# Kernel tuning notes

Hardware: AMD Instinct MI355X
Metric: run time of the kernel (lower is better)

## Reference

```python
import jax, jax.numpy as jnp
import numpy as np

H, W, C, R, N = 200, 200, 256, 1024, 300


def _mlp(f, W1, b1, W2, b2):
    # Linear -> ReLU -> Linear, applied per pixel
    return jax.nn.relu(f @ W1 + b1) @ W2 + b2


def setup_inputs() -> dict:
    key = jax.random.key(0)
    ks = jax.random.split(key, 16)
    s = 0.02
    inp = {
        'x': jax.random.normal(ks[0], (C, H, W), jnp.float32),
        'masks': jax.random.uniform(ks[1], (H, W, N)) < 0.5,
        'labels': jax.random.randint(ks[2], (N,), 0, 3),  # 0=point,1=line,2=circle
    }
    i = 3
    for p in ('p', 'l', 'c'):
        inp[f'W{p}1'] = s * jax.random.normal(ks[i], (C, R), jnp.float32); i += 1
        inp[f'b{p}1'] = jnp.zeros((R,), jnp.float32)
        inp[f'W{p}2'] = s * jax.random.normal(ks[i], (R, R), jnp.float32); i += 1
        inp[f'b{p}2'] = jnp.zeros((R,), jnp.float32)
    return inp


def reference(x, masks, labels, Wp1, bp1, Wp2, bp2, Wl1, bl1, Wl2, bl2, Wc1, bc1, Wc2, bc2):
    feat = jnp.transpose(x, (1, 2, 0))  # [H, W, C]
    # Apply each label-specific MLP densely over the feature map: [3, H, W, R]
    ys = jnp.stack([
        _mlp(feat, Wp1, bp1, Wp2, bp2),
        _mlp(feat, Wl1, bl1, Wl2, bl2),
        _mlp(feat, Wc1, bc1, Wc2, bc2),
    ], axis=0)
    mf = masks.astype(feat.dtype)                       # [H, W, N]
    sums = jnp.einsum('hwn,khwr->nkr', mf, ys)          # masked sums per node per MLP
    counts = jnp.sum(mf, axis=(0, 1))                   # [N] pixels per mask
    means = sums / counts[:, None, None]                # [N, 3, R]
    # pick the MLP branch matching each node's label -> [N, R]
    return means[jnp.arange(means.shape[0]), labels]
```

## Files before the change

### kernel.cpp

```cpp
#include <hip/hip_runtime.h>

typedef unsigned short u16;
typedef unsigned int   u32;

using bf16x8 = __attribute__((ext_vector_type(8))) __bf16;
using f32x4  = __attribute__((ext_vector_type(4))) float;

__device__ __forceinline__ float bf2f(u16 h){ return __uint_as_float(((u32)h) << 16); }
__device__ __forceinline__ u16 f2bf(float f){
    u32 u = __float_as_uint(f);
    u32 r = u + 0x7FFFu + ((u >> 16) & 1u);
    return (u16)(r >> 16);
}

__device__ __forceinline__ void async16(const void* g, void* l){
    __builtin_amdgcn_global_load_lds(
        (const __attribute__((address_space(1))) unsigned int*)g,
        (__attribute__((address_space(3))) unsigned int*)l, 16, 0, 0);
}
__device__ __forceinline__ bf16x8 cvt8(uint4 v){
    union { uint4 u; bf16x8 b; } c; c.u = v; return c.b;
}

__global__ void probe_and_perm(const void* x, const void* masks, int* flags,
                               const int* labels, int* slot_of_node,
                               int* node_of_slot, int* ovf_flag)
{
    if (blockIdx.x == 0){
        int l = threadIdx.x;
        if (l < 64){
            const u16* hx = (const u16*)x;
            int e0 = (hx[l] >> 7) & 0xFF;
            int e1 = (hx[l + 64] >> 7) & 0xFF;
            unsigned long long b0 = __ballot(e0 >= 100 && e0 <= 140);
            unsigned long long b1 = __ballot(e1 >= 100 && e1 <= 140);
            int cnt = __popcll(b0) + __popcll(b1);
            const u32* w  = (const u32*)masks;
            const u16* hm = (const u16*)masks;
            u32 v = w[l];
            unsigned long long i32bad = __ballot(v > 1u);
            unsigned long long f32bad = __ballot(v != 0u && v != 0x3F800000u);
            u16 h0 = hm[l], h1 = hm[l + 64];
            unsigned long long bfbad =
                __ballot((h0 != 0 && h0 != 0x3F80) || (h1 != 0 && h1 != 0x3F80));
            if (l == 0){
                flags[0] = (cnt >= 100) ? 1 : 0;
                int md = 0;
                if (!i32bad) md = 1; else if (!f32bad) md = 3; else if (!bfbad) md = 2;
                flags[1] = md;
            }
        }
        return;
    }
    __shared__ int lab[300];
    __shared__ unsigned char sp[300];
    int t = threadIdx.x;
    for (int idx = t; idx < 512; idx += 320) node_of_slot[idx] = -1;
    if (t < 300) lab[t] = labels[t];
    __syncthreads();
    int r = 0;
    if (t < 300){
        int k = lab[t];
        for (int j = 0; j < t; j++) r += (lab[j] == k);
        sp[t] = (r >= 128) ? 1 : 0;
    }
    __syncthreads();
    if (t < 300){
        int slot;
        if (!sp[t]) slot = lab[t] * 128 + r;
        else {
            int so = 0;
            for (int j = 0; j < t; j++) so += sp[j];
            slot = 384 + so;
        }
        slot_of_node[t] = slot;
        node_of_slot[slot] = t;
    }
    if (t == 0){
        int tot = 0;
        for (int j = 0; j < 300; j++) tot += sp[j];
        *ovf_flag = tot;
    }
}

__global__ void prep_combo(const void* x,
    const void* w10, const void* w11, const void* w12,
    const void* w20, const void* w21, const void* w22,
    const void* bb10, const void* bb11, const void* bb12,
    const void* bb20, const void* bb21, const void* bb22,
    u16* feat, u16* B1T, u16* W2T, float* b1f, float* b2f, const int* flags)
{
    __shared__ float tile[32][33];
    const int id = blockIdx.x;
    const bool isbf = (flags[0] != 0);
    const int tid = threadIdx.x;
    const int tx = tid & 31, ty = tid >> 5;

    const void* src; u16* d; int I, J, ldd, i0, j0;
    if (id < 10016){
        int fx = id % 1252, fy = id / 1252;
        src = x; d = feat; I = 256; J = 40000; ldd = 256;
        j0 = fx * 32; i0 = fy * 32;
    } else if (id < 10016 + 768){
        int idx = id - 10016;
        int z = idx / 256, r2 = idx % 256;
        src = (z == 0) ? w10 : (z == 1) ? w11 : w12;
        d = B1T + (size_t)z * 1024 * 256;
        I = 256; J = 1024; ldd = 256;
        j0 = (r2 % 32) * 32; i0 = (r2 / 32) * 32;
    } else if (id < 10016 + 768 + 3072){
        int idx = id - 10016 - 768;
        int z = idx / 1024, r2 = idx % 1024;
        src = (z == 0) ? w20 : (z == 1) ? w21 : w22;
        d = W2T + (size_t)z * 1024 * 1024;
        I = 1024; J = 1024; ldd = 1024;
        j0 = (r2 % 32) * 32; i0 = (r2 / 32) * 32;
    } else {
        int idx = (id - 10016 - 768 - 3072) * 256 + tid;
        if (idx < 3072){
            int k = idx >> 10, r2 = idx & 1023;
            const void* p1 = (k == 0) ? bb10 : (k == 1) ? bb11 : bb12;
            const void* p2 = (k == 0) ? bb20 : (k == 1) ? bb21 : bb22;
            b1f[idx] = isbf ? bf2f(((const u16*)p1)[r2]) : ((const float*)p1)[r2];
            b2f[idx] = isbf ? bf2f(((const u16*)p2)[r2]) : ((const float*)p2)[r2];
        }
        return;
    }
    #pragma unroll
    for (int s = 0; s < 32; s += 8){
        int i = i0 + ty + s, j = j0 + tx;
        float v = 0.f;
        if (j < J){
            size_t ix = (size_t)i * J + j;
            v = isbf ? bf2f(((const u16*)src)[ix]) : ((const float*)src)[ix];
        }
        tile[ty + s][tx] = v;
    }
    __syncthreads();
    #pragma unroll
    for (int s = 0; s < 32; s += 8){
        int j = j0 + ty + s, i = i0 + tx;
        d[(size_t)j * ldd + i] = f2bf(tile[tx][ty + s]);
    }
}

__global__ void trans_mask_count(const void* src, u16* dst,
                                 const int* slot_of_node, float* counts,
                                 const int* flags)
{
    constexpr int NN_ = 300, P_ = 40000, LDP = 40064;
    __shared__ u16 tile[128][33];
    __shared__ int slt[32];
    const int p0 = blockIdx.x * 128, n0 = blockIdx.y * 32;
    const int tid = threadIdx.x;
    const int md = flags[1];
    if (tid < 32) slt[tid] = (n0 + tid < NN_) ? slot_of_node[n0 + tid] : -1;

    if (md == 0){
        const unsigned char* s8 = (const unsigned char*)src;
        const int tx = tid & 7, ty = tid >> 3;
        #pragma unroll
        for (int rep = 0; rep < 4; rep++){
            const int p = p0 + rep * 32 + ty;
            const int nb = n0 + tx * 4;
            u32 w = 0;
            if (p < P_){
                if (nb + 3 < NN_)
                    w = *(const u32*)(s8 + (size_t)p * NN_ + nb);
                else {
                    for (int b = 0; b < 4; b++)
                        if (nb + b < NN_)
                            w |= (u32)s8[(size_t)p * NN_ + nb + b] << (8 * b);
                }
            }
            #pragma unroll
            for (int b = 0; b < 4; b++)
                tile[rep * 32 + ty][tx * 4 + b] =
                    ((w >> (8 * b)) & 0xFFu) ? (u16)0x3F80 : (u16)0;
        }
    } else {
        #pragma unroll
        for (int it = 0; it < 16; it++){
            const int e = tid + it * 256;
            const int n_in = e & 31, p_in = e >> 5;
            const int p = p0 + p_in, n = n0 + n_in;
            u16 v = 0;
            if (p < P_ && n < NN_){
                size_t idx = (size_t)p * NN_ + n;
                bool on;
                if (md == 1)      on = ((const int*)src)[idx] != 0;
                else if (md == 2) on = ((const u16*)src)[idx] != 0;
                else              on = ((const float*)src)[idx] != 0.f;
                v = on ? (u16)0x3F80 : (u16)0;
            }
            tile[p_in][n_in] = v;
        }
    }
    __syncthreads();

    #pragma unroll
    for (int half = 0; half < 2; half++){
        const int row = tid >> 3;
        const int pos = (tid & 7) + half * 8;
        const int slot = slt[row];
        if (slot >= 0){
            union { u16 h[8]; uint4 v; } tmp;
            #pragma unroll
            for (int j = 0; j < 8; j++) tmp.h[j] = tile[pos * 8 + j][row];
            *reinterpret_cast<uint4*>(&dst[(size_t)slot * LDP + p0 + pos * 8]) = tmp.v;
        }
    }
    if (tid < 32){
        const int slot = slt[tid];
        if (slot >= 0){
            int c = 0;
            for (int p = 0; p < 128; p++) c += (tile[p][tid] != 0);
            if (c > 0) atomicAdd(&counts[slot], (float)c);
        }
    }
}

template<int MAP>
__global__ __launch_bounds__(256, 2)
void fused_l1_mask(const u16* __restrict__ B1T, const u16* __restrict__ feat,
                   const u16* __restrict__ mfT, const float* __restrict__ b1f,
                   float* __restrict__ sums, const int* __restrict__ skipf)
{
    if constexpr (MAP == 1){ if (*skipf == 0) return; }
    constexpr int PPAD = 40064;
    __shared__ __align__(16) u16 As[32768];
    __shared__ __align__(16) u16 Hs[8192];

    int bx, ts, te;
    if constexpr (MAP == 0){
        const int id = blockIdx.x;
        const int r = id & 7, s = (id >> 3) & 7, g = id >> 6;
        const int combo = g * 8 + r;
        if (combo >= 63) return;
        const int branch = combo / 21, y = combo % 21;
        bx = branch * 8 + s;
        ts = y * 15; te = ts + 15; if (te > 313) te = 313;
    } else {
        bx = blockIdx.x;
        ts = blockIdx.y * 40; te = ts + 40; if (te > 313) te = 313;
        if (ts >= te) return;
    }
    const int m0 = bx * 128;
    const int srow = (MAP == 0) ? ((bx >> 3) * 128) : 384;

    const int tid = threadIdx.x;
    const int wave = tid >> 6, lane = tid & 63;
    const int t = lane & 15, q = lane >> 4;

    const int cr = lane >> 2, cp = lane & 3;
    const int ca = wave * 2, cb = wave * 2 + 1;
    {
        const u16* gA0 = B1T + (size_t)(m0 + ca * 16 + cr) * 256 + cp * 8;
        const u16* gA1 = B1T + (size_t)(m0 + cb * 16 + cr) * 256 + cp * 8;
        #pragma unroll
        for (int kt = 0; kt < 8; kt++){
            async16(gA0 + kt * 32, &As[kt * 4096 + ca * 512]);
            async16(gA1 + kt * 32, &As[kt * 4096 + cb * 512]);
        }
    }

    const u16* mrow = mfT + (size_t)(srow + wave*32 + t) * PPAD;
    const u16* gF   = feat + (size_t)(wave*32 + t) * 256 + q * 8;
    const float4* bsrc = reinterpret_cast<const float4*>(b1f + m0) + q;

    f32x4 acc2[2][8];
    #pragma unroll
    for (int a = 0; a < 2; a++)
        #pragma unroll
        for (int b = 0; b < 8; b++)
            #pragma unroll
            for (int e = 0; e < 4; e++) acc2[a][b][e] = 0.f;

    uint4 bgv[2];
    #pragma unroll
    for (int ni = 0; ni < 2; ni++)
        bgv[ni] = *reinterpret_cast<const uint4*>(
            gF + (size_t)(ts * 128 + ni * 16) * 256);

    __syncthreads();

    for (int pt = ts; pt < te; ++pt){
        const int p0 = pt * 128;

        f32x4 acc1[8][2];
        #pragma unroll
        for (int mi = 0; mi < 8; mi++){
            float4 bb = bsrc[mi * 4];
            #pragma unroll
            for (int ni = 0; ni < 2; ni++){
                acc1[mi][ni][0] = bb.x; acc1[mi][ni][1] = bb.y;
                acc1[mi][ni][2] = bb.z; acc1[mi][ni][3] = bb.w;
            }
        }

        uint4 ma0[2], ma1[2], mb0[2], mb1[2];

        #pragma unroll
        for (int kt = 0; kt < 8; ++kt){
            bf16x8 af[8];
            #pragma unroll
            for (int mi = 0; mi < 8; mi++)
                af[mi] = *reinterpret_cast<const bf16x8*>(
                    &As[kt*4096 + (mi*16 + t)*32 + q*8]);
            uint4 nxt[2];
            if (kt < 7){
                #pragma unroll
                for (int ni = 0; ni < 2; ni++)
                    nxt[ni] = *reinterpret_cast<const uint4*>(
                        gF + (size_t)(p0 + ni*16) * 256 + (kt + 1) * 32);
            } else {
                #pragma unroll
                for (int si = 0; si < 2; si++){
                    ma0[si] = *reinterpret_cast<const uint4*>(
                        mrow + (size_t)(si*16)*PPAD + p0 + 0*32 + q*8);
                    ma1[si] = *reinterpret_cast<const uint4*>(
                        mrow + (size_t)(si*16)*PPAD + p0 + 1*32 + q*8);
                }
            }
            #pragma unroll
            for (int mi = 0; mi < 8; mi++)
                #pragma unroll
                for (int ni = 0; ni < 2; ni++)
                    acc1[mi][ni] = __builtin_amdgcn_mfma_f32_16x16x32_bf16(
                        af[mi], cvt8(bgv[ni]), acc1[mi][ni], 0, 0, 0);
            if (kt < 7){
                #pragma unroll
                for (int ni = 0; ni < 2; ni++) bgv[ni] = nxt[ni];
            }
        }

        if (wave < 2){
            #pragma unroll
            for (int mi = 0; mi < 8; mi++){
                #pragma unroll
                for (int i = 0; i < 4; i++){
                    const int m_l = mi*16 + q*4 + i;
                    #pragma unroll
                    for (int ni = 0; ni < 2; ni++){
                        const int pin = ni*16 + t;
                        float v = acc1[mi][ni][i];
                        v = (v > 0.f) ? v : 0.f;
                        const int cg = (pin >> 3) ^ q;
                        Hs[wave*4096 + m_l*32 + cg*8 + (pin & 7)] = f2bf(v);
                    }
                }
            }
        }
        #pragma unroll
        for (int si = 0; si < 2; si++){
            mb0[si] = *reinterpret_cast<const uint4*>(
                mrow + (size_t)(si*16)*PPAD + p0 + 2*32 + q*8);
            mb1[si] = *reinterpret_cast<const uint4*>(
                mrow + (size_t)(si*16)*PPAD + p0 + 3*32 + q*8);
        }
        __syncthreads();

        #pragma unroll
        for (int lc = 0; lc < 2; lc++){
            const uint4* mm = (lc == 0) ? ma0 : ma1;
            bf16x8 hb[8];
            #pragma unroll
            for (int ni = 0; ni < 8; ni++)
                hb[ni] = *reinterpret_cast<const bf16x8*>(
                    &Hs[lc*4096 + (ni*16 + t)*32 + ((q ^ ((t >> 2) & 3)) * 8)]);
            #pragma unroll
            for (int si = 0; si < 2; si++)
                #pragma unroll
                for (int ni = 0; ni < 8; ni++)
                    acc2[si][ni] = __builtin_amdgcn_mfma_f32_16x16x32_bf16(
                        cvt8(mm[si]), hb[ni], acc2[si][ni], 0, 0, 0);
        }
        __syncthreads();

        if (wave >= 2){
            #pragma unroll
            for (int mi = 0; mi < 8; mi++){
                #pragma unroll
                for (int i = 0; i < 4; i++){
                    const int m_l = mi*16 + q*4 + i;
                    #pragma unroll
                    for (int ni = 0; ni < 2; ni++){
                        const int pin = ni*16 + t;
                        float v = acc1[mi][ni][i];
                        v = (v > 0.f) ? v : 0.f;
                        const int cg = (pin >> 3) ^ q;
                        Hs[(wave-2)*4096 + m_l*32 + cg*8 + (pin & 7)] = f2bf(v);
                    }
                }
            }
        }
        if (pt + 1 < te){
            #pragma unroll
            for (int ni = 0; ni < 2; ni++)
                bgv[ni] = *reinterpret_cast<const uint4*>(
                    gF + (size_t)((pt + 1) * 128 + ni * 16) * 256);
        }
        __syncthreads();

        #pragma unroll
        for (int lc = 0; lc < 2; lc++){
            const uint4* mm = (lc == 0) ? mb0 : mb1;
            bf16x8 hb[8];
            #pragma unroll
            for (int ni = 0; ni < 8; ni++)
                hb[ni] = *reinterpret_cast<const bf16x8*>(
                    &Hs[lc*4096 + (ni*16 + t)*32 + ((q ^ ((t >> 2) & 3)) * 8)]);
            #pragma unroll
            for (int si = 0; si < 2; si++)
                #pragma unroll
                for (int ni = 0; ni < 8; ni++)
                    acc2[si][ni] = __builtin_amdgcn_mfma_f32_16x16x32_bf16(
                        cvt8(mm[si]), hb[ni], acc2[si][ni], 0, 0, 0);
        }
        __syncthreads();
    }

    #pragma unroll
    for (int si = 0; si < 2; si++){
        #pragma unroll
        for (int i = 0; i < 4; i++){
            const int slot_l = wave*32 + si*16 + q*4 + i;
            #pragma unroll
            for (int ni = 0; ni < 8; ni++){
                const int m_l = ni*16 + t;
                const float v = acc2[si][ni][i];
                if constexpr (MAP == 0)
                    atomicAdd(sums + (size_t)((bx>>3)*128 + slot_l)*1024
                                   + (bx&7)*128 + m_l, v);
                else
                    atomicAdd(sums + (size_t)slot_l*3072 + bx*128 + m_l, v);
            }
        }
    }
}

__global__ __launch_bounds__(256)
void l2_gemm(const float* __restrict__ sums3, const float* __restrict__ sumsOvf,
             const float* __restrict__ counts, const u16* __restrict__ W2T,
             const float* __restrict__ b2f, const int* __restrict__ node_of_slot,
             const int* __restrict__ labels, const int* __restrict__ ovfflag,
             void* __restrict__ dout, const int* __restrict__ flags)
{
    const int z = blockIdx.z;
    const int k = (z >= 3) ? z - 3 : z;
    if (z >= 3 && *ovfflag == 0) return;
    const int n0 = blockIdx.x * 128;

    const float* Arow; int astride, slotbase;
    if (z < 3){ Arow = sums3 + (size_t)z * 128 * 1024; astride = 1024; slotbase = z * 128; }
    else      { Arow = sumsOvf + (size_t)k * 1024;     astride = 3072; slotbase = 384; }

    __shared__ __align__(16) u16 As[4096];
    __shared__ __align__(16) u16 Bs[4096];
    __shared__ float invc[128];

    const int tid  = threadIdx.x;
    const int wave = tid >> 6, lane = tid & 63;
    const int wr = wave >> 1, wc = wave & 1;
    const int t = lane & 15, q = lane >> 4;

    if (tid < 128){
        float c = counts[slotbase + tid];
        invc[tid] = (c > 0.f) ? 1.f / c : 0.f;
    }

    const u16* Bsrc = W2T + (size_t)k * 1024 * 1024;
    const int cr = lane >> 2, cp = lane & 3;
    const int ca = wave * 2, cb = wave * 2 + 1;
    const u16* gB0 = Bsrc + (size_t)(n0 + ca * 16 + cr) * 1024 + cp * 8;
    const u16* gB1 = Bsrc + (size_t)(n0 + cb * 16 + cr) * 1024 + cp * 8;

    f32x4 acc[4][4];
    #pragma unroll
    for (int a = 0; a < 4; a++)
        #pragma unroll
        for (int b = 0; b < 4; b++)
            #pragma unroll
            for (int e = 0; e < 4; e++) acc[a][b][e] = 0.f;

    for (int kt = 0; kt < 32; ++kt){
        __syncthreads();
        #pragma unroll
        for (int rep = 0; rep < 2; rep++){
            int idx = tid + rep * 256;
            int row = idx >> 2, quarter = idx & 3;
            const float4* src = reinterpret_cast<const float4*>(
                Arow + (size_t)row * astride + kt * 32 + quarter * 8);
            float4 v0 = src[0], v1 = src[1];
            float s = invc[row];
            union { u16 h[8]; uint4 v; } pk;
            pk.h[0] = f2bf(v0.x * s); pk.h[1] = f2bf(v0.y * s);
            pk.h[2] = f2bf(v0.z * s); pk.h[3] = f2bf(v0.w * s);
            pk.h[4] = f2bf(v1.x * s); pk.h[5] = f2bf(v1.y * s);
            pk.h[6] = f2bf(v1.z * s); pk.h[7] = f2bf(v1.w * s);
            *reinterpret_cast<uint4*>(&As[row * 32 + quarter * 8]) = pk.v;
        }
        async16(gB0 + kt * 32, Bs + ca * 512);
        async16(gB1 + kt * 32, Bs + cb * 512);
        __syncthreads();
        bf16x8 af[4], bg[4];
        #pragma unroll
        for (int mi = 0; mi < 4; mi++)
            af[mi] = *reinterpret_cast<const bf16x8*>(
                &As[(wr*64 + mi*16 + t)*32 + q*8]);
        #pragma unroll
        for (int ni = 0; ni < 4; ni++)
            bg[ni] = *reinterpret_cast<const bf16x8*>(
                &Bs[(wc*64 + ni*16 + t)*32 + q*8]);
        #pragma unroll
        for (int mi = 0; mi < 4; mi++)
            #pragma unroll
            for (int ni = 0; ni < 4; ni++)
                acc[mi][ni] = __builtin_amdgcn_mfma_f32_16x16x32_bf16(
                    af[mi], bg[ni], acc[mi][ni], 0, 0, 0);
    }

    const bool outbf = (flags[0] != 0);
    #pragma unroll
    for (int mi = 0; mi < 4; mi++){
        #pragma unroll
        for (int i = 0; i < 4; i++){
            int m_l = wr*64 + mi*16 + q*4 + i;
            int node = node_of_slot[slotbase + m_l];
            bool ok = (node >= 0) && (z < 3 || labels[node] == k);
            if (!ok) continue;
            #pragma unroll
            for (int ni = 0; ni < 4; ni++){
                int n = n0 + wc*64 + ni*16 + t;
                float v = acc[mi][ni][i] + b2f[k * 1024 + n];
                size_t oi = (size_t)node * 1024 + n;
                if (outbf) ((u16*)dout)[oi] = f2bf(v);
                else       ((float*)dout)[oi] = v;
            }
        }
    }
}

extern "C" void kernel_launch(void* const* d_in, const int* in_sizes, int n_in,
                              void* d_out, int out_size, void* d_ws, size_t ws_size,
                              hipStream_t stream)
{
    constexpr int C = 256, R = 1024;
    constexpr int PPAD = 40064;
    constexpr int M1 = 3 * R;
    constexpr int SLOTS = 512;

    const void* x      = d_in[0];
    const void* masks  = d_in[1];
    const int*  labels = (const int*)d_in[2];
    (void)in_sizes; (void)n_in; (void)out_size; (void)ws_size;

    char* ws = (char*)d_ws;
    size_t off = 0;
    auto alloc = [&](size_t b)->size_t {
        size_t o = off; off += (b + 255) & ~(size_t)255; return o;
    };

    int*   flags   = (int*)  (ws + alloc(256));
    int*   slotmap = (int*)  (ws + alloc(384 * 4));
    int*   nodemap = (int*)  (ws + alloc(512 * 4));
    int*   ovfflag = (int*)  (ws + alloc(256));
    u16*   feat    = (u16*)  (ws + alloc((size_t)PPAD * C * 2));
    u16*   B1T     = (u16*)  (ws + alloc((size_t)M1 * C * 2));
    float* b1f     = (float*)(ws + alloc((size_t)M1 * 4));
    float* b2f     = (float*)(ws + alloc((size_t)M1 * 4));
    u16*   mfT     = (u16*)  (ws + alloc((size_t)SLOTS * PPAD * 2));
    float* sums3   = (float*)(ws + alloc((size_t)384 * 1024 * 4));
    float* sumsOvf = (float*)(ws + alloc((size_t)128 * M1 * 4));
    float* counts  = (float*)(ws + alloc((size_t)SLOTS * 4));
    u16*   W2T     = (u16*)  (ws + alloc((size_t)3 * R * R * 2));

    probe_and_perm<<<2, 320, 0, stream>>>(x, masks, flags, labels,
                                          slotmap, nodemap, ovfflag);
    hipMemsetAsync(mfT, 0, (size_t)SLOTS * PPAD * 2, stream);
    hipMemsetAsync(sums3, 0,
        (size_t)384 * 1024 * 4 + (size_t)128 * M1 * 4 + (size_t)SLOTS * 4, stream);

    prep_combo<<<10016 + 768 + 3072 + 12, 256, 0, stream>>>(
        x, d_in[3], d_in[7], d_in[11],
        d_in[5], d_in[9], d_in[13],
        d_in[4], d_in[8], d_in[12],
        d_in[6], d_in[10], d_in[14],
        feat, B1T, W2T, b1f, b2f, flags);

    trans_mask_count<<<dim3(PPAD / 128, 384 / 32), 256, 0, stream>>>(
        masks, mfT, slotmap, counts, flags);

    fused_l1_mask<0><<<512, 256, 0, stream>>>(
        B1T, feat, mfT, b1f, sums3, nullptr);
    fused_l1_mask<1><<<dim3(24, 8), 256, 0, stream>>>(
        B1T, feat, mfT, b1f, sumsOvf, ovfflag);

    l2_gemm<<<dim3(8, 1, 6), 256, 0, stream>>>(
        sums3, sumsOvf, counts, W2T, b2f, nodemap, labels, ovfflag,
        d_out, flags);
}
```

Measured before the change: 378.7 us.

## Halve L1 tile to 64 rows, drop mfT memset, double-buffer L2 GEMM

The fused layer-1/mask kernel now works on 64-row weight tiles per block instead of 128. It uses a new 768-block mapping with 16 pixel chunks and 3 blocks per CU, and all four waves now write hidden activations in one phase instead of two. The layer-2 GEMM gets double-buffered LDS, prefetching the next A rows and the next B tile while the current tile runs through MFMA, and s_setprio raises priority around MFMA blocks. The memset of the transposed mask buffer is removed, which assumes every padded slot/pixel is written elsewhere, or garbage could leak into the sums. Smaller tiles halve feature reuse per block and double the atomic traffic into the sums.

```diff
diff --git a/kernel.cpp b/kernel.cpp
--- a/kernel.cpp
+++ b/kernel.cpp
@@ -221,58 +221,56 @@
 }
 
 template<int MAP>
-__global__ __launch_bounds__(256, 2)
+__global__ __launch_bounds__(256, 3)
 void fused_l1_mask(const u16* __restrict__ B1T, const u16* __restrict__ feat,
                    const u16* __restrict__ mfT, const float* __restrict__ b1f,
                    float* __restrict__ sums, const int* __restrict__ skipf)
 {
     if constexpr (MAP == 1){ if (*skipf == 0) return; }
     constexpr int PPAD = 40064;
-    __shared__ __align__(16) u16 As[32768];
+    __shared__ __align__(16) u16 As[16384];
     __shared__ __align__(16) u16 Hs[8192];
 
-    int bx, ts, te;
+    int branch, sm, ts, te;
     if constexpr (MAP == 0){
         const int id = blockIdx.x;
-        const int r = id & 7, s = (id >> 3) & 7, g = id >> 6;
-        const int combo = g * 8 + r;
-        if (combo >= 63) return;
-        const int branch = combo / 21, y = combo % 21;
-        bx = branch * 8 + s;
-        ts = y * 15; te = ts + 15; if (te > 313) te = 313;
+        const int r = id & 7, g = id >> 3;
+        sm = g & 15;
+        const int c = (g >> 4) * 8 + r;
+        branch = c >> 4;
+        const int y = c & 15;
+        ts = y * 19 + (y < 9 ? y : 9);
+        te = ts + 19 + (y < 9 ? 1 : 0);
     } else {
-        bx = blockIdx.x;
+        branch = 0;
+        sm = blockIdx.x;
         ts = blockIdx.y * 40; te = ts + 40; if (te > 313) te = 313;
         if (ts >= te) return;
     }
-    const int m0 = bx * 128;
-    const int srow = (MAP == 0) ? ((bx >> 3) * 128) : 384;
+    const int m0   = (MAP == 0) ? (branch * 1024 + sm * 64) : (sm * 64);
+    const int srow = (MAP == 0) ? (branch * 128) : 384;
 
     const int tid = threadIdx.x;
     const int wave = tid >> 6, lane = tid & 63;
     const int t = lane & 15, q = lane >> 4;
 
-    const int cr = lane >> 2, cp = lane & 3;
-    const int ca = wave * 2, cb = wave * 2 + 1;
     {
-        const u16* gA0 = B1T + (size_t)(m0 + ca * 16 + cr) * 256 + cp * 8;
-        const u16* gA1 = B1T + (size_t)(m0 + cb * 16 + cr) * 256 + cp * 8;
-        #pragma unroll
-        for (int kt = 0; kt < 8; kt++){
-            async16(gA0 + kt * 32, &As[kt * 4096 + ca * 512]);
-            async16(gA1 + kt * 32, &As[kt * 4096 + cb * 512]);
-        }
-    }
-
-    const u16* mrow = mfT + (size_t)(srow + wave*32 + t) * PPAD;
-    const u16* gF   = feat + (size_t)(wave*32 + t) * 256 + q * 8;
+        const u16* gA = B1T + (size_t)(m0 + wave * 16 + (lane >> 2)) * 256
+                        + (lane & 3) * 8;
+        #pragma unroll
+        for (int kt = 0; kt < 8; kt++)
+            async16(gA + kt * 32, &As[kt * 2048 + wave * 512]);
+    }
+
+    const u16* mrow = mfT + (size_t)(srow + wave * 32 + t) * PPAD;
+    const u16* gF   = feat + (size_t)(wave * 32 + t) * 256 + q * 8;
     const float4* bsrc = reinterpret_cast<const float4*>(b1f + m0) + q;
 
-    f32x4 acc2[2][8];
+    f32x4 acc2[2][4];
     #pragma unroll
     for (int a = 0; a < 2; a++)
         #pragma unroll
-        for (int b = 0; b < 8; b++)
+        for (int b = 0; b < 4; b++)
             #pragma unroll
             for (int e = 0; e < 4; e++) acc2[a][b][e] = 0.f;
 
@@ -287,9 +285,9 @@
     for (int pt = ts; pt < te; ++pt){
         const int p0 = pt * 128;
 
-        f32x4 acc1[8][2];
-        #pragma unroll
-        for (int mi = 0; mi < 8; mi++){
+        f32x4 acc1[4][2];
+        #pragma unroll
+        for (int mi = 0; mi < 4; mi++){
             float4 bb = bsrc[mi * 4];
             #pragma unroll
             for (int ni = 0; ni < 2; ni++){
@@ -298,142 +296,105 @@
             }
         }
 
-        uint4 ma0[2], ma1[2], mb0[2], mb1[2];
+        uint4 mA[4];
 
         #pragma unroll
         for (int kt = 0; kt < 8; ++kt){
-            bf16x8 af[8];
-            #pragma unroll
-            for (int mi = 0; mi < 8; mi++)
+            bf16x8 af[4];
+            #pragma unroll
+            for (int mi = 0; mi < 4; mi++)
                 af[mi] = *reinterpret_cast<const bf16x8*>(
-                    &As[kt*4096 + (mi*16 + t)*32 + q*8]);
+                    &As[kt * 2048 + (mi * 16 + t) * 32 + q * 8]);
             uint4 nxt[2];
             if (kt < 7){
                 #pragma unroll
                 for (int ni = 0; ni < 2; ni++)
                     nxt[ni] = *reinterpret_cast<const uint4*>(
-                        gF + (size_t)(p0 + ni*16) * 256 + (kt + 1) * 32);
+                        gF + (size_t)(p0 + ni * 16) * 256 + (kt + 1) * 32);
             } else {
                 #pragma unroll
-                for (int si = 0; si < 2; si++){
-                    ma0[si] = *reinterpret_cast<const uint4*>(
-                        mrow + (size_t)(si*16)*PPAD + p0 + 0*32 + q*8);
-                    ma1[si] = *reinterpret_cast<const uint4*>(
-                        mrow + (size_t)(si*16)*PPAD + p0 + 1*32 + q*8);
-                }
-            }
-            #pragma unroll
-            for (int mi = 0; mi < 8; mi++)
+                for (int lc = 0; lc < 2; lc++)
+                    #pragma unroll
+                    for (int si = 0; si < 2; si++)
+                        mA[lc * 2 + si] = *reinterpret_cast<const uint4*>(
+                            mrow + (size_t)(si * 16) * PPAD + p0 + lc * 32 + q * 8);
+            }
+            __builtin_amdgcn_s_setprio(1);
+            #pragma unroll
+            for (int mi = 0; mi < 4; mi++)
                 #pragma unroll
                 for (int ni = 0; ni < 2; ni++)
                     acc1[mi][ni] = __builtin_amdgcn_mfma_f32_16x16x32_bf16(
                         af[mi], cvt8(bgv[ni]), acc1[mi][ni], 0, 0, 0);
-            if (kt < 7){
+            __builtin_amdgcn_s_setprio(0);
+            if (kt < 7){ bgv[0] = nxt[0]; bgv[1] = nxt[1]; }
+        }
+
+        #pragma unroll
+        for (int mi = 0; mi < 4; mi++){
+            #pragma unroll
+            for (int i = 0; i < 4; i++){
+                const int m_l = mi * 16 + q * 4 + i;
                 #pragma unroll
-                for (int ni = 0; ni < 2; ni++) bgv[ni] = nxt[ni];
-            }
-        }
-
-        if (wave < 2){
-            #pragma unroll
-            for (int mi = 0; mi < 8; mi++){
-                #pragma unroll
-                for (int i = 0; i < 4; i++){
-                    const int m_l = mi*16 + q*4 + i;
-                    #pragma unroll
-                    for (int ni = 0; ni < 2; ni++){
-                        const int pin = ni*16 + t;
-                        float v = acc1[mi][ni][i];
-                        v = (v > 0.f) ? v : 0.f;
-                        const int cg = (pin >> 3) ^ q;
-                        Hs[wave*4096 + m_l*32 + cg*8 + (pin & 7)] = f2bf(v);
-                    }
+                for (int ni = 0; ni < 2; ni++){
+                    const int pin = ni * 16 + t;
+                    float v = acc1[mi][ni][i];
+                    v = (v > 0.f) ? v : 0.f;
+                    const int cg = (pin >> 3) ^ q;
+                    Hs[wave * 2048 + m_l * 32 + cg * 8 + (pin & 7)] = f2bf(v);
                 }
             }
         }
-        #pragma unroll
-        for (int si = 0; si < 2; si++){
-            mb0[si] = *reinterpret_cast<const uint4*>(
-                mrow + (size_t)(si*16)*PPAD + p0 + 2*32 + q*8);
-            mb1[si] = *reinterpret_cast<const uint4*>(
-                mrow + (size_t)(si*16)*PPAD + p0 + 3*32 + q*8);
-        }
         __syncthreads();
 
-        #pragma unroll
-        for (int lc = 0; lc < 2; lc++){
-            const uint4* mm = (lc == 0) ? ma0 : ma1;
-            bf16x8 hb[8];
-            #pragma unroll
-            for (int ni = 0; ni < 8; ni++)
+        uint4 mB[4];
+        #pragma unroll
+        for (int lc = 0; lc < 2; lc++)
+            #pragma unroll
+            for (int si = 0; si < 2; si++)
+                mB[lc * 2 + si] = *reinterpret_cast<const uint4*>(
+                    mrow + (size_t)(si * 16) * PPAD + p0 + (lc + 2) * 32 + q * 8);
+
+        #pragma unroll
+        for (int lc = 0; lc < 4; lc++){
+            const uint4* mm = (lc < 2) ? &mA[lc * 2] : &mB[(lc - 2) * 2];
+            bf16x8 hb[4];
+            #pragma unroll
+            for (int ni = 0; ni < 4; ni++)
                 hb[ni] = *reinterpret_cast<const bf16x8*>(
-                    &Hs[lc*4096 + (ni*16 + t)*32 + ((q ^ ((t >> 2) & 3)) * 8)]);
+                    &Hs[lc * 2048 + (ni * 16 + t) * 32 + ((q ^ ((t >> 2) & 3)) * 8)]);
+            __builtin_amdgcn_s_setprio(1);
             #pragma unroll
             for (int si = 0; si < 2; si++)
                 #pragma unroll
-                for (int ni = 0; ni < 8; ni++)
+                for (int ni = 0; ni < 4; ni++)
                     acc2[si][ni] = __builtin_amdgcn_mfma_f32_16x16x32_bf16(
                         cvt8(mm[si]), hb[ni], acc2[si][ni], 0, 0, 0);
+            __builtin_amdgcn_s_setprio(0);
+            if (lc == 1 && pt + 1 < te){
+                #pragma unroll
+                for (int ni = 0; ni < 2; ni++)
+                    bgv[ni] = *reinterpret_cast<const uint4*>(
+                        gF + (size_t)((pt + 1) * 128 + ni * 16) * 256);
+            }
         }
         __syncthreads();
-
-        if (wave >= 2){
-            #pragma unroll
-            for (int mi = 0; mi < 8; mi++){
-                #pragma unroll
-                for (int i = 0; i < 4; i++){
-                    const int m_l = mi*16 + q*4 + i;
-                    #pragma unroll
-                    for (int ni = 0; ni < 2; ni++){
-                        const int pin = ni*16 + t;
-                        float v = acc1[mi][ni][i];
-                        v = (v > 0.f) ? v : 0.f;
-                        const int cg = (pin >> 3) ^ q;
-                        Hs[(wave-2)*4096 + m_l*32 + cg*8 + (pin & 7)] = f2bf(v);
-                    }
-                }
-            }
-        }
-        if (pt + 1 < te){
-            #pragma unroll
-            for (int ni = 0; ni < 2; ni++)
-                bgv[ni] = *reinterpret_cast<const uint4*>(
-                    gF + (size_t)((pt + 1) * 128 + ni * 16) * 256);
-        }
-        __syncthreads();
-
-        #pragma unroll
-        for (int lc = 0; lc < 2; lc++){
-            const uint4* mm = (lc == 0) ? mb0 : mb1;
-            bf16x8 hb[8];
-            #pragma unroll
-            for (int ni = 0; ni < 8; ni++)
-                hb[ni] = *reinterpret_cast<const bf16x8*>(
-                    &Hs[lc*4096 + (ni*16 + t)*32 + ((q ^ ((t >> 2) & 3)) * 8)]);
-            #pragma unroll
-            for (int si = 0; si < 2; si++)
-                #pragma unroll
-                for (int ni = 0; ni < 8; ni++)
-                    acc2[si][ni] = __builtin_amdgcn_mfma_f32_16x16x32_bf16(
-                        cvt8(mm[si]), hb[ni], acc2[si][ni], 0, 0, 0);
-        }
-        __syncthreads();
     }
 
     #pragma unroll
     for (int si = 0; si < 2; si++){
         #pragma unroll
         for (int i = 0; i < 4; i++){
-            const int slot_l = wave*32 + si*16 + q*4 + i;
-            #pragma unroll
-            for (int ni = 0; ni < 8; ni++){
-                const int m_l = ni*16 + t;
+            const int slot_l = wave * 32 + si * 16 + q * 4 + i;
+            #pragma unroll
+            for (int ni = 0; ni < 4; ni++){
+                const int m_l = ni * 16 + t;
                 const float v = acc2[si][ni][i];
                 if constexpr (MAP == 0)
-                    atomicAdd(sums + (size_t)((bx>>3)*128 + slot_l)*1024
-                                   + (bx&7)*128 + m_l, v);
+                    atomicAdd(sums + (size_t)(branch * 128 + slot_l) * 1024
+                                   + sm * 64 + m_l, v);
                 else
-                    atomicAdd(sums + (size_t)slot_l*3072 + bx*128 + m_l, v);
+                    atomicAdd(sums + (size_t)slot_l * 3072 + sm * 64 + m_l, v);
             }
         }
     }
@@ -455,8 +416,8 @@
     if (z < 3){ Arow = sums3 + (size_t)z * 128 * 1024; astride = 1024; slotbase = z * 128; }
     else      { Arow = sumsOvf + (size_t)k * 1024;     astride = 3072; slotbase = 384; }
 
-    __shared__ __align__(16) u16 As[4096];
-    __shared__ __align__(16) u16 Bs[4096];
+    __shared__ __align__(16) u16 As[2][4096];
+    __shared__ __align__(16) u16 Bs[2][4096];
     __shared__ float invc[128];
 
     const int tid  = threadIdx.x;
@@ -468,6 +429,7 @@
         float c = counts[slotbase + tid];
         invc[tid] = (c > 0.f) ? 1.f / c : 0.f;
     }
+    __syncthreads();
 
     const u16* Bsrc = W2T + (size_t)k * 1024 * 1024;
     const int cr = lane >> 2, cp = lane & 3;
@@ -475,6 +437,39 @@
     const u16* gB0 = Bsrc + (size_t)(n0 + ca * 16 + cr) * 1024 + cp * 8;
     const u16* gB1 = Bsrc + (size_t)(n0 + cb * 16 + cr) * 1024 + cp * 8;
 
+    const int srow0 = tid >> 2, sq0 = tid & 3;
+    const int srow1 = srow0 + 64;
+
+    float4 sv[2][2];
+
+#define L2_LOAD(ktv) do{ \
+    const float4* _p0 = reinterpret_cast<const float4*>( \
+        Arow + (size_t)srow0 * astride + (ktv) * 32 + sq0 * 8); \
+    const float4* _p1 = reinterpret_cast<const float4*>( \
+        Arow + (size_t)srow1 * astride + (ktv) * 32 + sq0 * 8); \
+    sv[0][0] = _p0[0]; sv[0][1] = _p0[1]; \
+    sv[1][0] = _p1[0]; sv[1][1] = _p1[1]; }while(0)
+
+#define L2_WRITE(bufv) do{ \
+    _Pragma("unroll") \
+    for (int rep = 0; rep < 2; rep++){ \
+        const int row = (rep == 0) ? srow0 : srow1; \
+        const float s = invc[row]; \
+        float4 v0 = sv[rep][0], v1 = sv[rep][1]; \
+        union { u16 h[8]; uint4 v; } pk; \
+        pk.h[0] = f2bf(v0.x * s); pk.h[1] = f2bf(v0.y * s); \
+        pk.h[2] = f2bf(v0.z * s); pk.h[3] = f2bf(v0.w * s); \
+        pk.h[4] = f2bf(v1.x * s); pk.h[5] = f2bf(v1.y * s); \
+        pk.h[6] = f2bf(v1.z * s); pk.h[7] = f2bf(v1.w * s); \
+        *reinterpret_cast<uint4*>(&As[bufv][row * 32 + sq0 * 8]) = pk.v; \
+    } }while(0)
+
+    L2_LOAD(0);
+    L2_WRITE(0);
+    async16(gB0, &Bs[0][ca * 512]);
+    async16(gB1, &Bs[0][cb * 512]);
+    __syncthreads();
+
     f32x4 acc[4][4];
     #pragma unroll
     for (int a = 0; a < 4; a++)
@@ -483,55 +478,49 @@
             #pragma unroll
             for (int e = 0; e < 4; e++) acc[a][b][e] = 0.f;
 
+    int buf = 0;
     for (int kt = 0; kt < 32; ++kt){
-        __syncthreads();
-        #pragma unroll
-        for (int rep = 0; rep < 2; rep++){
-            int idx = tid + rep * 256;
-            int row = idx >> 2, quarter = idx & 3;
-            const float4* src = reinterpret_cast<const float4*>(
-                Arow + (size_t)row * astride + kt * 32 + quarter * 8);
-            float4 v0 = src[0], v1 = src[1];
-            float s = invc[row];
-            union { u16 h[8]; uint4 v; } pk;
-            pk.h[0] = f2bf(v0.x * s); pk.h[1] = f2bf(v0.y * s);
-            pk.h[2] = f2bf(v0.z * s); pk.h[3] = f2bf(v0.w * s);
-            pk.h[4] = f2bf(v1.x * s); pk.h[5] = f2bf(v1.y * s);
-            pk.h[6] = f2bf(v1.z * s); pk.h[7] = f2bf(v1.w * s);
-            *reinterpret_cast<uint4*>(&As[row * 32 + quarter * 8]) = pk.v;
-        }
-        async16(gB0 + kt * 32, Bs + ca * 512);
-        async16(gB1 + kt * 32, Bs + cb * 512);
-        __syncthreads();
+        if (kt < 31) L2_LOAD(kt + 1);
         bf16x8 af[4], bg[4];
         #pragma unroll
         for (int mi = 0; mi < 4; mi++)
             af[mi] = *reinterpret_cast<const bf16x8*>(
-                &As[(wr*64 + mi*16 + t)*32 + q*8]);
+                &As[buf][(wr * 64 + mi * 16 + t) * 32 + q * 8]);
         #pragma unroll
         for (int ni = 0; ni < 4; ni++)
             bg[ni] = *reinterpret_cast<const bf16x8*>(
-                &Bs[(wc*64 + ni*16 + t)*32 + q*8]);
+                &Bs[buf][(wc * 64 + ni * 16 + t) * 32 + q * 8]);
+        if (kt < 31){
+            async16(gB0 + (kt + 1) * 32, &Bs[buf ^ 1][ca * 512]);
+            async16(gB1 + (kt + 1) * 32, &Bs[buf ^ 1][cb * 512]);
+        }
+        __builtin_amdgcn_s_setprio(1);
         #pragma unroll
         for (int mi = 0; mi < 4; mi++)
             #pragma unroll
             for (int ni = 0; ni < 4; ni++)
                 acc[mi][ni] = __builtin_amdgcn_mfma_f32_16x16x32_bf16(
                     af[mi], bg[ni], acc[mi][ni], 0, 0, 0);
-    }
+        __builtin_amdgcn_s_setprio(0);
+        if (kt < 31) L2_WRITE(buf ^ 1);
+        __syncthreads();
+        buf ^= 1;
+    }
+#undef L2_LOAD
+#undef L2_WRITE
 
     const bool outbf = (flags[0] != 0);
     #pragma unroll
     for (int mi = 0; mi < 4; mi++){
         #pragma unroll
         for (int i = 0; i < 4; i++){
-            int m_l = wr*64 + mi*16 + q*4 + i;
+            int m_l = wr * 64 + mi * 16 + q * 4 + i;
             int node = node_of_slot[slotbase + m_l];
             bool ok = (node >= 0) && (z < 3 || labels[node] == k);
             if (!ok) continue;
             #pragma unroll
             for (int ni = 0; ni < 4; ni++){
-                int n = n0 + wc*64 + ni*16 + t;
+                int n = n0 + wc * 64 + ni * 16 + t;
                 float v = acc[mi][ni][i] + b2f[k * 1024 + n];
                 size_t oi = (size_t)node * 1024 + n;
                 if (outbf) ((u16*)dout)[oi] = f2bf(v);
@@ -577,7 +566,6 @@
 
     probe_and_perm<<<2, 320, 0, stream>>>(x, masks, flags, labels,
                                           slotmap, nodemap, ovfflag);
-    hipMemsetAsync(mfT, 0, (size_t)SLOTS * PPAD * 2, stream);
     hipMemsetAsync(sums3, 0,
         (size_t)384 * 1024 * 4 + (size_t)128 * M1 * 4 + (size_t)SLOTS * 4, stream);
 
@@ -591,9 +579,9 @@
     trans_mask_count<<<dim3(PPAD / 128, 384 / 32), 256, 0, stream>>>(
         masks, mfT, slotmap, counts, flags);
 
-    fused_l1_mask<0><<<512, 256, 0, stream>>>(
+    fused_l1_mask<0><<<768, 256, 0, stream>>>(
         B1T, feat, mfT, b1f, sums3, nullptr);
-    fused_l1_mask<1><<<dim3(24, 8), 256, 0, stream>>>(
+    fused_l1_mask<1><<<dim3(48, 8), 256, 0, stream>>>(
         B1T, feat, mfT, b1f, sumsOvf, ovfflag);
 
     l2_gemm<<<dim3(8, 1, 6), 256, 0, stream>>>(
```

After: 548.8 us. +44.9%, slower.
